# Optimization experiments

Hardware: AMD Instinct MI355X
Metric: run time of the kernel (lower is better)

The kernel has to match this reference:

```python
import jax, jax.numpy as jnp
import numpy as np
import math

D = 512
B, L = 8, 2048
EPS = 1e-5

def setup_inputs() -> dict:
    key = jax.random.key(0)
    ks = jax.random.split(key, 8)
    s = 1.0 / math.sqrt(D)
    x = jax.random.normal(ks[0], (B, L, D), dtype=jnp.float32)
    adj = jax.random.randint(ks[1], (B, L, L), 0, 2, dtype=jnp.int32)
    Wq = jax.random.normal(ks[2], (D, D), dtype=jnp.float32) * s
    Wk = jax.random.normal(ks[3], (D, D), dtype=jnp.float32) * s
    Wv = jax.random.normal(ks[4], (D, D), dtype=jnp.float32) * s
    Wo = jax.random.normal(ks[5], (D, D), dtype=jnp.float32) * s
    bo = jnp.zeros((D,), dtype=jnp.float32)
    gamma = jnp.ones((D,), dtype=jnp.float32)
    beta = jnp.zeros((D,), dtype=jnp.float32)
    return {"x": x, "adj": adj, "Wq": Wq, "Wk": Wk, "Wv": Wv,
            "Wo": Wo, "bo": bo, "gamma": gamma, "beta": beta}

def layer_norm(y, gamma, beta):
    mu = jnp.mean(y, axis=-1, keepdims=True)
    var = jnp.mean(jnp.square(y - mu), axis=-1, keepdims=True)
    return (y - mu) * jax.lax.rsqrt(var + EPS) * gamma + beta

def reference(x, adj, Wq, Wk, Wv, Wo, bo, gamma, beta):
    d_out = Wq.shape[1]
    scale = 1.0 / math.sqrt(d_out)
    Q = x @ Wq                          # [B,L,D]
    K = x @ Wk
    V = x @ Wv
    sc = jnp.einsum('bld,bmd->blm', Q, K) * scale   # [B,L,L]
    mask = adj == 0
    sc = jnp.where(mask, -jnp.inf, sc)
    all_inf = jnp.all(mask, axis=-1, keepdims=True)  # rows with no neighbors
    sc = jnp.where(all_inf, 0.0, sc)                 # -> uniform attention
    w = jax.nn.softmax(sc, axis=-1)                  # dropout off (eval)
    out = jnp.einsum('blm,bmd->bld', w, V)
    y = x + out @ Wo + bo
    return layer_norm(y, gamma, beta)
```

## Files before the change

### kernel.cpp

```cpp
#include <hip/hip_runtime.h>
#include <hip/hip_bf16.h>

typedef short bf16x8 __attribute__((ext_vector_type(8)));
typedef float f32x4  __attribute__((ext_vector_type(4)));
typedef unsigned int u32;

#define LSEQ 2048
#define DDIM 512
#define NBAT 8

__device__ __forceinline__ void gld_lds16(const void* g, void* l) {
    __builtin_amdgcn_global_load_lds(
        (const __attribute__((address_space(1))) u32*)g,
        (__attribute__((address_space(3))) u32*)l, 16, 0, 0);
}
__device__ __forceinline__ float bf2f(short s) {
    u32 u = ((u32)(unsigned short)s) << 16;
    union { u32 u; float f; } c; c.u = u; return c.f;
}
__device__ __forceinline__ short f2bf(float f) {
    __hip_bfloat16 h = __float2bfloat16(f);
    return *(short*)&h;
}

__global__ void k_cvt(const float* __restrict__ x, const float* __restrict__ Wq,
                      const float* __restrict__ Wk, const float* __restrict__ Wv,
                      const float* __restrict__ Wo, __hip_bfloat16* __restrict__ xb,
                      __hip_bfloat16* __restrict__ Wtqkv, __hip_bfloat16* __restrict__ Wto) {
    __shared__ float t[32][33];
    if (blockIdx.x < 1024) {
        int mat = blockIdx.x >> 8;
        int tb  = blockIdx.x & 255;
        int tk  = tb >> 4, tn = tb & 15;
        const float* W = (mat == 0) ? Wq : (mat == 1) ? Wk : (mat == 2) ? Wv : Wo;
        int c  = threadIdx.x & 31;
        int r0 = threadIdx.x >> 5;
#pragma unroll
        for (int i = 0; i < 4; ++i) {
            int r = r0 + i * 8;
            t[r][c] = W[(size_t)(tk * 32 + r) * 512 + tn * 32 + c];
        }
        __syncthreads();
        __hip_bfloat16* dst = (mat < 3) ? (Wtqkv + (size_t)mat * 512 * 512) : Wto;
#pragma unroll
        for (int i = 0; i < 4; ++i) {
            int n = r0 + i * 8;
            dst[(size_t)(tn * 32 + n) * 512 + tk * 32 + c] = __float2bfloat16(t[c][n]);
        }
    } else {
        size_t i = ((size_t)(blockIdx.x - 1024) * 256 + threadIdx.x) * 4;
        float4 v = *(const float4*)(x + i);
        __hip_bfloat16 h[4] = { __float2bfloat16(v.x), __float2bfloat16(v.y),
                                __float2bfloat16(v.z), __float2bfloat16(v.w) };
        *(short4*)(xb + i) = *(short4*)h;
    }
}

__global__ __launch_bounds__(256, 2)
void k_gemm_qkv(const __hip_bfloat16* __restrict__ A, const __hip_bfloat16* __restrict__ Bt,
                __hip_bfloat16* __restrict__ Q, __hip_bfloat16* __restrict__ Kb,
                __hip_bfloat16* __restrict__ Vt) {
    __shared__ __hip_bfloat16 As[128][32], Bs[128][32];
    const int tid = threadIdx.x, lane = tid & 63, w = tid >> 6;
    const int l15 = lane & 15, l4 = lane >> 4;
    const int mt = blockIdx.x, nt = blockIdx.y;
    const int wr = (w >> 1) * 64, wc = (w & 1) * 64;
    const int sr = lane >> 2, so = (lane & 3) * 8;
    f32x4 acc[4][4] = {};

#pragma unroll 1
    for (int kt = 0; kt < 16; ++kt) {
        __syncthreads();
#pragma unroll
        for (int i = 0; i < 2; ++i) {
            int r0 = w * 32 + i * 16;
            gld_lds16(A  + (size_t)(mt * 128 + r0 + sr) * 512 + kt * 32 + so, &As[r0][0]);
            gld_lds16(Bt + (size_t)(nt * 128 + r0 + sr) * 512 + kt * 32 + so, &Bs[r0][0]);
        }
        __syncthreads();
        bf16x8 af[4], bfr[4];
#pragma unroll
        for (int i = 0; i < 4; ++i)
            af[i] = *(const bf16x8*)(&As[wr + 16 * i + l15][l4 * 8]);
#pragma unroll
        for (int j = 0; j < 4; ++j)
            bfr[j] = *(const bf16x8*)(&Bs[wc + 16 * j + l15][l4 * 8]);
        __builtin_amdgcn_s_setprio(1);
#pragma unroll
        for (int i = 0; i < 4; ++i)
#pragma unroll
            for (int j = 0; j < 4; ++j)
                acc[i][j] = __builtin_amdgcn_mfma_f32_16x16x32_bf16(af[i], bfr[j], acc[i][j], 0, 0, 0);
        __builtin_amdgcn_s_setprio(0);
    }
    const int which = (nt * 128) >> 9;
#pragma unroll
    for (int i = 0; i < 4; ++i) {
#pragma unroll
        for (int r = 0; r < 4; ++r) {
            int grow = mt * 128 + wr + 16 * i + (l4 << 2) + r;
#pragma unroll
            for (int j = 0; j < 4; ++j) {
                int gcol = nt * 128 + wc + 16 * j + l15;
                int cc = gcol & 511;
                __hip_bfloat16 h = __float2bfloat16(acc[i][j][r]);
                if (which == 0)      Q [(size_t)grow * 512 + cc] = h;
                else if (which == 1) Kb[(size_t)grow * 512 + cc] = h;
                else {
                    int b = grow >> 11, m = grow & 2047;
                    Vt[((size_t)b * 512 + cc) * 2048 + m] = h;
                }
            }
        }
    }
}

__global__ __launch_bounds__(512, 2)
void k_attn(const __hip_bfloat16* __restrict__ Q, const __hip_bfloat16* __restrict__ Kg,
            const __hip_bfloat16* __restrict__ Vt, const int* __restrict__ adj,
            __hip_bfloat16* __restrict__ P0, __hip_bfloat16* __restrict__ P1,
            float* __restrict__ mlb) {
    __shared__ __hip_bfloat16 Kl[2][32][520];
    __shared__ __hip_bfloat16 Vl[2][512][32];
    __shared__ __hip_bfloat16 Pl[8][16][40];
    const int tid = threadIdx.x, lane = tid & 63, w = tid >> 6;
    const int l15 = lane & 15, l4 = lane >> 4;
    const int b = blockIdx.x & 7, qt = (blockIdx.x >> 3) & 15, s = blockIdx.x >> 7;
    const float scale = 0.04419417382415922f;
    __hip_bfloat16* __restrict__ Op = s ? P1 : P0;

    const __hip_bfloat16* kbase = Kg + ((size_t)b * LSEQ + s * 1024) * 512;
    const __hip_bfloat16* vbase = Vt + (size_t)b * 512 * 2048 + s * 1024;
    const int* abase = adj + ((size_t)b * LSEQ + qt * 128 + w * 16 + l4 * 4) * LSEQ + s * 1024 + l15;
    const int vsr = lane >> 2;
    const int vswz = (l4 ^ ((l15 >> 1) & 3)) * 8;

    bf16x8 qf[16];
    {
        const __hip_bfloat16* qp = Q + ((size_t)b * LSEQ + qt * 128 + w * 16 + l15) * 512;
#pragma unroll
        for (int ks = 0; ks < 16; ++ks)
            qf[ks] = *(const bf16x8*)(qp + ks * 32 + l4 * 8);
    }
    f32x4 acc[32];
#pragma unroll
    for (int n = 0; n < 32; ++n) acc[n] = (f32x4){0.f, 0.f, 0.f, 0.f};
    float m_[4] = {-1e30f, -1e30f, -1e30f, -1e30f};
    float l_[4] = {0.f, 0.f, 0.f, 0.f};

    int adjv[8];
    {
#pragma unroll
        for (int i = 0; i < 4; ++i) {
            int r = w + i * 8;
            gld_lds16(kbase + (size_t)r * 512 + lane * 8, &Kl[0][r][0]);
        }
#pragma unroll
        for (int i = 0; i < 4; ++i) {
            int r0 = (w * 4 + i) * 16;
            int d  = r0 + vsr;
            gld_lds16(vbase + (size_t)d * 2048 + (((lane & 3) ^ ((d >> 1) & 3)) << 3), &Vl[0][r0][0]);
        }
#pragma unroll
        for (int r = 0; r < 4; ++r)
#pragma unroll
            for (int n = 0; n < 2; ++n)
                adjv[r * 2 + n] = abase[(size_t)r * LSEQ + n * 16];
    }
    __syncthreads();

#pragma unroll 1
    for (int t = 0; t < 32; ++t) {
        const int cur = t & 1, nxt = cur ^ 1;
        unsigned amask = 0;
#pragma unroll
        for (int r = 0; r < 4; ++r)
#pragma unroll
            for (int n = 0; n < 2; ++n)
                amask |= (adjv[r * 2 + n] != 0 ? 1u : 0u) << (n * 4 + r);
        if (t < 31) {
            const __hip_bfloat16* kp = kbase + (size_t)(t + 1) * 32 * 512;
#pragma unroll
            for (int i = 0; i < 4; ++i) {
                int r = w + i * 8;
                gld_lds16(kp + (size_t)r * 512 + lane * 8, &Kl[nxt][r][0]);
            }
            const __hip_bfloat16* vp = vbase + (t + 1) * 32;
#pragma unroll
            for (int i = 0; i < 4; ++i) {
                int r0 = (w * 4 + i) * 16;
                int d  = r0 + vsr;
                gld_lds16(vp + (size_t)d * 2048 + (((lane & 3) ^ ((d >> 1) & 3)) << 3), &Vl[nxt][r0][0]);
            }
            const int* ap = abase + (t + 1) * 32;
#pragma unroll
            for (int r = 0; r < 4; ++r)
#pragma unroll
                for (int n = 0; n < 2; ++n)
                    adjv[r * 2 + n] = ap[(size_t)r * LSEQ + n * 16];
        }
        f32x4 sa[2];
#pragma unroll
        for (int n = 0; n < 2; ++n) sa[n] = (f32x4){0.f, 0.f, 0.f, 0.f};
        __builtin_amdgcn_s_setprio(1);
#pragma unroll
        for (int ks = 0; ks < 16; ++ks) {
#pragma unroll
            for (int n = 0; n < 2; ++n) {
                bf16x8 bk = *(const bf16x8*)(&Kl[cur][n * 16 + l15][ks * 32 + l4 * 8]);
                sa[n] = __builtin_amdgcn_mfma_f32_16x16x32_bf16(qf[ks], bk, sa[n], 0, 0, 0);
            }
        }
        __builtin_amdgcn_s_setprio(0);
        float mx[4];
#pragma unroll
        for (int r = 0; r < 4; ++r) {
            float v = -1e30f;
#pragma unroll
            for (int n = 0; n < 2; ++n)
                if ((amask >> (n * 4 + r)) & 1) v = fmaxf(v, sa[n][r] * scale);
            v = fmaxf(v, __shfl_xor(v, 1));
            v = fmaxf(v, __shfl_xor(v, 2));
            v = fmaxf(v, __shfl_xor(v, 4));
            v = fmaxf(v, __shfl_xor(v, 8));
            mx[r] = v;
        }
        float rs[4];
        bool need = false;
#pragma unroll
        for (int r = 0; r < 4; ++r) {
            rs[r] = 1.f;
            if (mx[r] > m_[r] + 8.f) { rs[r] = __expf(m_[r] - mx[r]); m_[r] = mx[r]; }
            l_[r] *= rs[r];
            need |= (rs[r] != 1.f);
        }
        if (need) {
#pragma unroll
            for (int n = 0; n < 32; ++n) {
                acc[n][0] *= rs[0]; acc[n][1] *= rs[1];
                acc[n][2] *= rs[2]; acc[n][3] *= rs[3];
            }
        }
#pragma unroll
        for (int n = 0; n < 2; ++n)
#pragma unroll
            for (int r = 0; r < 4; ++r) {
                float p = ((amask >> (n * 4 + r)) & 1) ? __expf(sa[n][r] * scale - m_[r]) : 0.f;
                sa[n][r] = p;
            }
#pragma unroll
        for (int r = 0; r < 4; ++r) {
            float sm = sa[0][r] + sa[1][r];
            sm += __shfl_xor(sm, 1);
            sm += __shfl_xor(sm, 2);
            sm += __shfl_xor(sm, 4);
            sm += __shfl_xor(sm, 8);
            l_[r] += sm;
        }
#pragma unroll
        for (int n = 0; n < 2; ++n)
#pragma unroll
            for (int r = 0; r < 4; ++r)
                Pl[w][l4 * 4 + r][n * 16 + l15] = __float2bfloat16(sa[n][r]);
        {
            bf16x8 pf = *(const bf16x8*)(&Pl[w][l15][l4 * 8]);
            __builtin_amdgcn_s_setprio(1);
#pragma unroll
            for (int n = 0; n < 32; ++n) {
                bf16x8 bv = *(const bf16x8*)(&Vl[cur][n * 16 + l15][vswz]);
                acc[n] = __builtin_amdgcn_mfma_f32_16x16x32_bf16(pf, bv, acc[n], 0, 0, 0);
            }
            __builtin_amdgcn_s_setprio(0);
        }
        __syncthreads();
    }
#pragma unroll
    for (int r = 0; r < 4; ++r) {
        size_t row = (size_t)b * LSEQ + qt * 128 + w * 16 + l4 * 4 + r;
#pragma unroll
        for (int n = 0; n < 32; ++n)
            Op[row * 512 + n * 16 + l15] = __float2bfloat16(acc[n][r]);
        if (l15 == 0) {
            mlb[((size_t)s * 16384 + row) * 2 + 0] = m_[r];
            mlb[((size_t)s * 16384 + row) * 2 + 1] = l_[r];
        }
    }
}

__global__ __launch_bounds__(512, 2)
void k_out_ln(const __hip_bfloat16* __restrict__ p0, const __hip_bfloat16* __restrict__ p1,
              const float* __restrict__ mlb, const __hip_bfloat16* __restrict__ Bt,
              const float* __restrict__ x, const float* __restrict__ bo,
              const float* __restrict__ gamma, const float* __restrict__ beta,
              float* __restrict__ out) {
    __shared__ __hip_bfloat16 As[64][32];
    __shared__ __hip_bfloat16 Bs[512][32];
    __shared__ float part[64][4][2];
    __shared__ float lnmv[64][2];
    const int tid = threadIdx.x, lane = tid & 63, w = tid >> 6;
    const int l15 = lane & 15, l4 = lane >> 4;
    const int mt = blockIdx.x;
    const int rs = (w >> 2) * 32, cbs = (w & 3) * 128;
    f32x4 acc[2][8] = {};

    float c0 = 0.f, c1 = 0.f;
    size_t grow_s = 0;
    int ko = (tid & 3) * 8;
    if (tid < 256) {
        int arow = tid >> 2;
        grow_s = (size_t)mt * 64 + arow;
        float m0 = mlb[grow_s * 2], l0 = mlb[grow_s * 2 + 1];
        float m1 = mlb[(16384 + grow_s) * 2], l1 = mlb[(16384 + grow_s) * 2 + 1];
        float M  = fmaxf(m0, m1);
        float e0 = __expf(m0 - M), e1 = __expf(m1 - M);
        float den = l0 * e0 + l1 * e1;
        float inv = (den > 0.f) ? 1.f / den : 0.f;
        c0 = e0 * inv; c1 = e1 * inv;
    }

#pragma unroll 1
    for (int kt = 0; kt < 16; ++kt) {
        __syncthreads();
#pragma unroll
        for (int i = 0; i < 4; ++i) {
            int br = w * 64 + i * 16;
            gld_lds16(Bt + (size_t)(br + (lane >> 2)) * 512 + kt * 32 + (lane & 3) * 8, &Bs[br][0]);
        }
        if (tid < 256) {
            bf16x8 a0 = *(const bf16x8*)(p0 + grow_s * 512 + kt * 32 + ko);
            bf16x8 a1 = *(const bf16x8*)(p1 + grow_s * 512 + kt * 32 + ko);
            short h[8];
#pragma unroll
            for (int k = 0; k < 8; ++k)
                h[k] = f2bf(c0 * bf2f(((short*)&a0)[k]) + c1 * bf2f(((short*)&a1)[k]));
            *(bf16x8*)(&As[tid >> 2][ko]) = *(bf16x8*)h;
        }
        __syncthreads();
        bf16x8 af[2], bfr[8];
#pragma unroll
        for (int i = 0; i < 2; ++i)
            af[i] = *(const bf16x8*)(&As[rs + 16 * i + l15][l4 * 8]);
#pragma unroll
        for (int j = 0; j < 8; ++j)
            bfr[j] = *(const bf16x8*)(&Bs[cbs + 16 * j + l15][l4 * 8]);
        __builtin_amdgcn_s_setprio(1);
#pragma unroll
        for (int i = 0; i < 2; ++i)
#pragma unroll
            for (int j = 0; j < 8; ++j)
                acc[i][j] = __builtin_amdgcn_mfma_f32_16x16x32_bf16(af[i], bfr[j], acc[i][j], 0, 0, 0);
        __builtin_amdgcn_s_setprio(0);
    }
#pragma unroll
    for (int i = 0; i < 2; ++i) {
#pragma unroll
        for (int r = 0; r < 4; ++r) {
            int rl = rs + 16 * i + 4 * l4 + r;
            size_t grow = (size_t)mt * 64 + rl;
            float s = 0.f, q = 0.f;
#pragma unroll
            for (int j = 0; j < 8; ++j) {
                int col = cbs + 16 * j + l15;
                float y = x[grow * 512 + col] + acc[i][j][r] + bo[col];
                acc[i][j][r] = y;
                s += y; q += y * y;
            }
            s += __shfl_xor(s, 1); q += __shfl_xor(q, 1);
            s += __shfl_xor(s, 2); q += __shfl_xor(q, 2);
            s += __shfl_xor(s, 4); q += __shfl_xor(q, 4);
            s += __shfl_xor(s, 8); q += __shfl_xor(q, 8);
            if (l15 == 0) { part[rl][w & 3][0] = s; part[rl][w & 3][1] = q; }
        }
    }
    __syncthreads();
    if (tid < 64) {
        float S  = part[tid][0][0] + part[tid][1][0] + part[tid][2][0] + part[tid][3][0];
        float Q2 = part[tid][0][1] + part[tid][1][1] + part[tid][2][1] + part[tid][3][1];
        float mu = S * (1.f / 512.f);
        float var = Q2 * (1.f / 512.f) - mu * mu;
        lnmv[tid][0] = mu;
        lnmv[tid][1] = rsqrtf(var + 1e-5f);
    }
    __syncthreads();
    float gm[8], bt2[8];
#pragma unroll
    for (int j = 0; j < 8; ++j) {
        int col = cbs + 16 * j + l15;
        gm[j] = gamma[col]; bt2[j] = beta[col];
    }
#pragma unroll
    for (int i = 0; i < 2; ++i) {
#pragma unroll
        for (int r = 0; r < 4; ++r) {
            int rl = rs + 16 * i + 4 * l4 + r;
            size_t grow = (size_t)mt * 64 + rl;
            float mu = lnmv[rl][0], rsd = lnmv[rl][1];
#pragma unroll
            for (int j = 0; j < 8; ++j) {
                int col = cbs + 16 * j + l15;
                out[grow * 512 + col] = (acc[i][j][r] - mu) * rsd * gm[j] + bt2[j];
            }
        }
    }
}

extern "C" void kernel_launch(void* const* d_in, const int* in_sizes, int n_in,
                              void* d_out, int out_size, void* d_ws, size_t ws_size,
                              hipStream_t stream) {
    const float* x     = (const float*)d_in[0];
    const int*   adj   = (const int*)d_in[1];
    const float* Wq    = (const float*)d_in[2];
    const float* Wk    = (const float*)d_in[3];
    const float* Wv    = (const float*)d_in[4];
    const float* Wo    = (const float*)d_in[5];
    const float* bo    = (const float*)d_in[6];
    const float* gamma = (const float*)d_in[7];
    const float* beta  = (const float*)d_in[8];
    float* out = (float*)d_out;

    char* ws = (char*)d_ws;
    const size_t SZ_ROWS = (size_t)NBAT * LSEQ;
    __hip_bfloat16* xb    = (__hip_bfloat16*)(ws);
    __hip_bfloat16* Wtqkv = (__hip_bfloat16*)(ws + 16777216);
    __hip_bfloat16* Wto   = (__hip_bfloat16*)(ws + 18350080);
    __hip_bfloat16* Qb    = (__hip_bfloat16*)(ws + 18874368);
    __hip_bfloat16* Kb    = (__hip_bfloat16*)(ws + 35651584);
    __hip_bfloat16* Vtb   = (__hip_bfloat16*)(ws + 52428800);
    __hip_bfloat16* P1    = (__hip_bfloat16*)(ws + 69206016);
    float*          mlb   = (float*)         (ws + 85983232);
    __hip_bfloat16* P0    = xb;
    (void)in_sizes; (void)n_in; (void)out_size; (void)ws_size;

    k_cvt<<<1024 + (unsigned)((SZ_ROWS * DDIM) / (256 * 4)), 256, 0, stream>>>(
        x, Wq, Wk, Wv, Wo, xb, Wtqkv, Wto);
    k_gemm_qkv<<<dim3(128, 12), 256, 0, stream>>>(xb, Wtqkv, Qb, Kb, Vtb);
    k_attn<<<256, 512, 0, stream>>>(Qb, Kb, Vtb, adj, P0, P1, mlb);
    k_out_ln<<<256, 512, 0, stream>>>(P0, P1, mlb, Wto, x, bo, gamma, beta, out);
}
```

Before: 236.5 us.

## Double-buffer LDS tiles in QKV and output-projection GEMM kernels

Both the QKV projection GEMM and the output-projection+LayerNorm GEMM now keep two LDS stages. Each iteration issues the next K-tile's global-to-LDS loads (and in k_out_ln, the global loads for the split-combine of the A tile) before the current tile's MFMAs, leaving one barrier per iteration instead of two. This is meant to hide global-load latency behind compute. The cost is double the LDS footprint, which may lower occupancy, particularly for k_out_ln with its 512x32 B tile.

```diff
diff --git a/kernel.cpp b/kernel.cpp
--- a/kernel.cpp
+++ b/kernel.cpp
@@ -60,7 +60,7 @@
 void k_gemm_qkv(const __hip_bfloat16* __restrict__ A, const __hip_bfloat16* __restrict__ Bt,
                 __hip_bfloat16* __restrict__ Q, __hip_bfloat16* __restrict__ Kb,
                 __hip_bfloat16* __restrict__ Vt) {
-    __shared__ __hip_bfloat16 As[128][32], Bs[128][32];
+    __shared__ __hip_bfloat16 As[2][128][32], Bs[2][128][32];
     const int tid = threadIdx.x, lane = tid & 63, w = tid >> 6;
     const int l15 = lane & 15, l4 = lane >> 4;
     const int mt = blockIdx.x, nt = blockIdx.y;
@@ -68,23 +68,32 @@
     const int sr = lane >> 2, so = (lane & 3) * 8;
     f32x4 acc[4][4] = {};
 
+#pragma unroll
+    for (int i = 0; i < 2; ++i) {
+        int r0 = w * 32 + i * 16;
+        gld_lds16(A  + (size_t)(mt * 128 + r0 + sr) * 512 + so, &As[0][r0][0]);
+        gld_lds16(Bt + (size_t)(nt * 128 + r0 + sr) * 512 + so, &Bs[0][r0][0]);
+    }
+    __syncthreads();
+
 #pragma unroll 1
     for (int kt = 0; kt < 16; ++kt) {
-        __syncthreads();
-#pragma unroll
-        for (int i = 0; i < 2; ++i) {
-            int r0 = w * 32 + i * 16;
-            gld_lds16(A  + (size_t)(mt * 128 + r0 + sr) * 512 + kt * 32 + so, &As[r0][0]);
-            gld_lds16(Bt + (size_t)(nt * 128 + r0 + sr) * 512 + kt * 32 + so, &Bs[r0][0]);
-        }
-        __syncthreads();
+        const int cur = kt & 1, nxt = cur ^ 1;
+        if (kt < 15) {
+#pragma unroll
+            for (int i = 0; i < 2; ++i) {
+                int r0 = w * 32 + i * 16;
+                gld_lds16(A  + (size_t)(mt * 128 + r0 + sr) * 512 + (kt + 1) * 32 + so, &As[nxt][r0][0]);
+                gld_lds16(Bt + (size_t)(nt * 128 + r0 + sr) * 512 + (kt + 1) * 32 + so, &Bs[nxt][r0][0]);
+            }
+        }
         bf16x8 af[4], bfr[4];
 #pragma unroll
         for (int i = 0; i < 4; ++i)
-            af[i] = *(const bf16x8*)(&As[wr + 16 * i + l15][l4 * 8]);
+            af[i] = *(const bf16x8*)(&As[cur][wr + 16 * i + l15][l4 * 8]);
 #pragma unroll
         for (int j = 0; j < 4; ++j)
-            bfr[j] = *(const bf16x8*)(&Bs[wc + 16 * j + l15][l4 * 8]);
+            bfr[j] = *(const bf16x8*)(&Bs[cur][wc + 16 * j + l15][l4 * 8]);
         __builtin_amdgcn_s_setprio(1);
 #pragma unroll
         for (int i = 0; i < 4; ++i)
@@ -92,6 +101,7 @@
             for (int j = 0; j < 4; ++j)
                 acc[i][j] = __builtin_amdgcn_mfma_f32_16x16x32_bf16(af[i], bfr[j], acc[i][j], 0, 0, 0);
         __builtin_amdgcn_s_setprio(0);
+        __syncthreads();
     }
     const int which = (nt * 128) >> 9;
 #pragma unroll
@@ -293,8 +303,8 @@
               const float* __restrict__ x, const float* __restrict__ bo,
               const float* __restrict__ gamma, const float* __restrict__ beta,
               float* __restrict__ out) {
-    __shared__ __hip_bfloat16 As[64][32];
-    __shared__ __hip_bfloat16 Bs[512][32];
+    __shared__ __hip_bfloat16 As[2][64][32];
+    __shared__ __hip_bfloat16 Bs[2][512][32];
     __shared__ float part[64][4][2];
     __shared__ float lnmv[64][2];
     const int tid = threadIdx.x, lane = tid & 63, w = tid >> 6;
@@ -318,31 +328,45 @@
         c0 = e0 * inv; c1 = e1 * inv;
     }
 
+#pragma unroll
+    for (int i = 0; i < 4; ++i) {
+        int br = w * 64 + i * 16;
+        gld_lds16(Bt + (size_t)(br + (lane >> 2)) * 512 + (lane & 3) * 8, &Bs[0][br][0]);
+    }
+    if (tid < 256) {
+        bf16x8 a0 = *(const bf16x8*)(p0 + grow_s * 512 + ko);
+        bf16x8 a1 = *(const bf16x8*)(p1 + grow_s * 512 + ko);
+        short h[8];
+#pragma unroll
+        for (int k = 0; k < 8; ++k)
+            h[k] = f2bf(c0 * bf2f(((short*)&a0)[k]) + c1 * bf2f(((short*)&a1)[k]));
+        *(bf16x8*)(&As[0][tid >> 2][ko]) = *(bf16x8*)h;
+    }
+    __syncthreads();
+
 #pragma unroll 1
     for (int kt = 0; kt < 16; ++kt) {
-        __syncthreads();
-#pragma unroll
-        for (int i = 0; i < 4; ++i) {
-            int br = w * 64 + i * 16;
-            gld_lds16(Bt + (size_t)(br + (lane >> 2)) * 512 + kt * 32 + (lane & 3) * 8, &Bs[br][0]);
-        }
-        if (tid < 256) {
-            bf16x8 a0 = *(const bf16x8*)(p0 + grow_s * 512 + kt * 32 + ko);
-            bf16x8 a1 = *(const bf16x8*)(p1 + grow_s * 512 + kt * 32 + ko);
-            short h[8];
-#pragma unroll
-            for (int k = 0; k < 8; ++k)
-                h[k] = f2bf(c0 * bf2f(((short*)&a0)[k]) + c1 * bf2f(((short*)&a1)[k]));
-            *(bf16x8*)(&As[tid >> 2][ko]) = *(bf16x8*)h;
-        }
-        __syncthreads();
+        const int cur = kt & 1, nxt = cur ^ 1;
+        bf16x8 a0, a1;
+        if (kt < 15) {
+#pragma unroll
+            for (int i = 0; i < 4; ++i) {
+                int br = w * 64 + i * 16;
+                gld_lds16(Bt + (size_t)(br + (lane >> 2)) * 512 + (kt + 1) * 32 + (lane & 3) * 8,
+                          &Bs[nxt][br][0]);
+            }
+            if (tid < 256) {
+                a0 = *(const bf16x8*)(p0 + grow_s * 512 + (kt + 1) * 32 + ko);
+                a1 = *(const bf16x8*)(p1 + grow_s * 512 + (kt + 1) * 32 + ko);
+            }
+        }
         bf16x8 af[2], bfr[8];
 #pragma unroll
         for (int i = 0; i < 2; ++i)
-            af[i] = *(const bf16x8*)(&As[rs + 16 * i + l15][l4 * 8]);
+            af[i] = *(const bf16x8*)(&As[cur][rs + 16 * i + l15][l4 * 8]);
 #pragma unroll
         for (int j = 0; j < 8; ++j)
-            bfr[j] = *(const bf16x8*)(&Bs[cbs + 16 * j + l15][l4 * 8]);
+            bfr[j] = *(const bf16x8*)(&Bs[cur][cbs + 16 * j + l15][l4 * 8]);
         __builtin_amdgcn_s_setprio(1);
 #pragma unroll
         for (int i = 0; i < 2; ++i)
@@ -350,6 +374,14 @@
             for (int j = 0; j < 8; ++j)
                 acc[i][j] = __builtin_amdgcn_mfma_f32_16x16x32_bf16(af[i], bfr[j], acc[i][j], 0, 0, 0);
         __builtin_amdgcn_s_setprio(0);
+        if (kt < 15 && tid < 256) {
+            short h[8];
+#pragma unroll
+            for (int k = 0; k < 8; ++k)
+                h[k] = f2bf(c0 * bf2f(((short*)&a0)[k]) + c1 * bf2f(((short*)&a1)[k]));
+            *(bf16x8*)(&As[nxt][tid >> 2][ko]) = *(bf16x8*)h;
+        }
+        __syncthreads();
     }
 #pragma unroll
     for (int i = 0; i < 2; ++i) {
```

Result: no change. 234.2 us, median of 2 (-0.9%).
